# Performance work log

Hardware: AMD Instinct MI355X
Metric: run time of the kernel (lower is better)

Reference implementation:

```python
import jax, jax.numpy as jnp
import numpy as np

N_NODES = 131072
N_EDGES = 2097152
N_GRAPHS = 16384
LRELU_ATT = 0.2   # GATConv negative_slope
LRELU_ACT = 0.01  # F.leaky_relu default
BN_EPS = 1e-5


def _gat_layer(x, src, dst, edge_attr, W, a_src, a_dst, We, a_edge, b, H, C, concat, n_nodes):
    # x: [N, Fin]; W: [Fin, H*C]; a_src/a_dst/a_edge: [H, C]; We: [1, H*C]; b: [H*C] or [C]
    h = (x @ W).reshape(-1, H, C)                                   # [N, H, C]
    alpha_src = jnp.einsum('nhc,hc->nh', h, a_src)                  # [N, H]
    alpha_dst = jnp.einsum('nhc,hc->nh', h, a_dst)                  # [N, H]
    he = (edge_attr @ We).reshape(-1, H, C)                          # [E, H, C]
    alpha_e = jnp.einsum('ehc,hc->eh', he, a_edge)                   # [E, H]
    alpha = alpha_src[src] + alpha_dst[dst] + alpha_e                # [E, H]
    alpha = jax.nn.leaky_relu(alpha, LRELU_ATT)
    # edge-softmax over destination nodes (numerically stable)
    amax = jax.ops.segment_max(alpha, dst, num_segments=n_nodes)
    ex = jnp.exp(alpha - amax[dst])
    denom = jax.ops.segment_sum(ex, dst, num_segments=n_nodes)
    att = ex / (denom[dst] + 1e-16)                                  # [E, H]
    out = jax.ops.segment_sum(h[src] * att[:, :, None], dst, num_segments=n_nodes)  # [N, H, C]
    out = out.reshape(n_nodes, H * C) if concat else out.mean(axis=1)
    return out + b


def setup_inputs() -> dict:
    key = jax.random.key(0)
    ks = iter(jax.random.split(key, 64))
    d = {}
    d['x'] = jax.random.normal(next(ks), (N_NODES, 6), dtype=jnp.float32)
    d['edge_index'] = jax.random.randint(next(ks), (2, N_EDGES), 0, N_NODES, dtype=jnp.int32)
    d['edge_weight'] = jax.random.uniform(next(ks), (N_EDGES,), dtype=jnp.float32)
    d['batch'] = jnp.sort(jax.random.randint(next(ks), (N_NODES,), 0, N_GRAPHS, dtype=jnp.int32))
    # GAT layers: (in, out_channels, heads)
    cfgs = [(6, 16, 4), (64, 32, 4), (128, 16, 4), (64, 50, 1)]
    for i, (fin, C, H) in enumerate(cfgs, 1):
        s = 1.0 / np.sqrt(fin)
        d[f'W{i}'] = jax.random.normal(next(ks), (fin, H * C), dtype=jnp.float32) * s
        d[f'as{i}'] = jax.random.normal(next(ks), (H, C), dtype=jnp.float32) * (1.0 / np.sqrt(C))
        d[f'ad{i}'] = jax.random.normal(next(ks), (H, C), dtype=jnp.float32) * (1.0 / np.sqrt(C))
        d[f'We{i}'] = jax.random.normal(next(ks), (1, H * C), dtype=jnp.float32)
        d[f'ae{i}'] = jax.random.normal(next(ks), (H, C), dtype=jnp.float32) * (1.0 / np.sqrt(C))
        out_dim = H * C if i < 4 else C  # concat for 1-3, not layer 4
        d[f'b{i}'] = jnp.zeros((out_dim,), dtype=jnp.float32)
    d['bn_g'] = jnp.ones((50,), dtype=jnp.float32)
    d['bn_b'] = jnp.zeros((50,), dtype=jnp.float32)
    d['bn_rm'] = jax.random.normal(next(ks), (50,), dtype=jnp.float32) * 0.1
    d['bn_rv'] = jnp.abs(jax.random.normal(next(ks), (50,), dtype=jnp.float32)) + 0.5
    for name, (fi, fo) in [('f1', (50, 30)), ('f2', (30, 20)), ('f3', (20, 2))]:
        d[f'W{name}'] = jax.random.normal(next(ks), (fi, fo), dtype=jnp.float32) * (1.0 / np.sqrt(fi))
        d[f'b{name}'] = jnp.zeros((fo,), dtype=jnp.float32)
    return d


def reference(x, edge_index, edge_weight, batch,
              W1, as1, ad1, We1, ae1, b1,
              W2, as2, ad2, We2, ae2, b2,
              W3, as3, ad3, We3, ae3, b3,
              W4, as4, ad4, We4, ae4, b4,
              bn_g, bn_b, bn_rm, bn_rv,
              Wf1, bf1, Wf2, bf2, Wf3, bf3):
    src, dst = edge_index[0], edge_index[1]
    ea = edge_weight[:, None]  # edge_dim = 1
    n = x.shape[0]
    h = jax.nn.leaky_relu(_gat_layer(x, src, dst, ea, W1, as1, ad1, We1, ae1, b1, 4, 16, True, n), LRELU_ACT)
    h = jax.nn.leaky_relu(_gat_layer(h, src, dst, ea, W2, as2, ad2, We2, ae2, b2, 4, 32, True, n), LRELU_ACT)
    h = jax.nn.leaky_relu(_gat_layer(h, src, dst, ea, W3, as3, ad3, We3, ae3, b3, 4, 16, True, n), LRELU_ACT)
    h = _gat_layer(h, src, dst, ea, W4, as4, ad4, We4, ae4, b4, 1, 50, False, n)
    # BatchNorm (eval mode: running stats)
    h = (h - bn_rm) * jax.lax.rsqrt(bn_rv + BN_EPS) * bn_g + bn_b
    h = jax.nn.leaky_relu(h, LRELU_ACT)
    g = jax.ops.segment_sum(h, batch, num_segments=N_GRAPHS)  # global_add_pool
    g = jax.nn.leaky_relu(g @ Wf1 + bf1, LRELU_ACT)  # dropout p=0.2 is a no-op in eval
    g = jax.nn.leaky_relu(g @ Wf2 + bf2, LRELU_ACT)
    return g @ Wf3 + bf3
```

## Files before the change

### kernel.cpp

```cpp
#include <hip/hip_runtime.h>
#include <hip/hip_fp16.h>
#include <math.h>

#define NN 131072
#define NE 2097152
#define NG 16384

__device__ __forceinline__ float lrelu(float x, float s) { return fmaxf(x, s * x); }

template <int H>
__device__ __forceinline__ float sel_h(const float* a, int hsel) {
    if constexpr (H == 1) return a[0];
    else return hsel == 0 ? a[0] : hsel == 1 ? a[1] : hsel == 2 ? a[2] : a[3];
}

__global__ void k_hist(const int* __restrict__ dst, int* __restrict__ cnt, int* __restrict__ rank) {
    int e = blockIdx.x * 256 + threadIdx.x;
    rank[e] = atomicAdd(&cnt[dst[e]], 1);
}

__global__ void k_scan1(const int* __restrict__ cnt, int* __restrict__ rowptr, int* __restrict__ part) {
    __shared__ int s[256];
    int t = threadIdx.x;
    int i = blockIdx.x * 256 + t;
    int v = cnt[i];
    s[t] = v;
    __syncthreads();
    for (int off = 1; off < 256; off <<= 1) {
        int x = (t >= off) ? s[t - off] : 0;
        __syncthreads();
        s[t] += x;
        __syncthreads();
    }
    rowptr[i] = s[t] - v;
    if (t == 255) part[blockIdx.x] = s[255];
}

__global__ void k_scan2(int* part,
                        const float* __restrict__ We1, const float* __restrict__ ae1,
                        const float* __restrict__ We2, const float* __restrict__ ae2,
                        const float* __restrict__ We3, const float* __restrict__ ae3,
                        const float* __restrict__ We4, const float* __restrict__ ae4,
                        float* __restrict__ ceb) {
    __shared__ int s[512];
    int t = threadIdx.x;
    int v = part[t];
    s[t] = v;
    __syncthreads();
    for (int off = 1; off < 512; off <<= 1) {
        int x = (t >= off) ? s[t - off] : 0;
        __syncthreads();
        s[t] += x;
        __syncthreads();
    }
    part[t] = s[t] - v;
    if (t < 4) {
        float c = 0.f;
        for (int i = 0; i < 16; i++) c += We1[t * 16 + i] * ae1[t * 16 + i];
        ceb[t] = c;
    } else if (t < 8) {
        int h = t - 4;
        float c = 0.f;
        for (int i = 0; i < 32; i++) c += We2[h * 32 + i] * ae2[h * 32 + i];
        ceb[t] = c;
    } else if (t < 12) {
        int h = t - 8;
        float c = 0.f;
        for (int i = 0; i < 16; i++) c += We3[h * 16 + i] * ae3[h * 16 + i];
        ceb[t] = c;
    } else if (t == 12) {
        float c = 0.f;
        for (int i = 0; i < 50; i++) c += We4[i] * ae4[i];
        ceb[t] = c;
    }
}

__global__ void k_scan3(int* __restrict__ rowptr, const int* __restrict__ part) {
    int t = threadIdx.x;
    int i = blockIdx.x * 256 + t;
    rowptr[i] = rowptr[i] + part[blockIdx.x];
    if (i == 0) rowptr[NN] = NE;
}

__global__ void k_scatter(const int* __restrict__ src, const int* __restrict__ dst,
                          const float* __restrict__ ew, const int* __restrict__ rowptr,
                          const int* __restrict__ rank, unsigned int* __restrict__ ep) {
    int e = blockIdx.x * 256 + threadIdx.x;
    int d = dst[e];
    int p = rowptr[d] + rank[e];
    unsigned int s = (unsigned int)src[e];
    unsigned int q = (unsigned int)(ew[e] * 32767.f + 0.5f);
    __builtin_nontemporal_store((s << 15) | (q & 0x7fffu), &ep[p]);
}

__device__ __forceinline__ void ep_unpack(unsigned int u, int& s, float& w) {
    s = (int)(u >> 15);
    w = (float)(u & 0x7fffu) * (1.f / 32767.f);
}

template <int FIN, int F, int FR, int H, int C, int ITER>
__global__ __launch_bounds__(256) void k_transform(
    const float* __restrict__ in, const float* __restrict__ W,
    const float* __restrict__ as_, const float* __restrict__ ad_,
    __half* __restrict__ h, float* __restrict__ alpha_s, float* __restrict__ alpha_d) {
    constexpr int TF = F / 16;
    constexpr int XS = 65;
    __shared__ float Wl[FIN * F];
    __shared__ float Xl[FIN * XS];
    int t = threadIdx.x;
    int tfg = t & 15;
    int ng = t >> 4;
    int f0 = tfg * TF;

    for (int i = t; i < FIN * F; i += 256) {
        int ff = i % F;
        Wl[i] = (ff < FR) ? W[(i / F) * FR + ff] : 0.f;
    }
    float asf[TF], adf[TF];
#pragma unroll
    for (int j = 0; j < TF; j++) {
        bool v = (f0 + j) < FR;
        asf[j] = v ? as_[f0 + j] : 0.f;
        adf[j] = v ? ad_[f0 + j] : 0.f;
    }

    for (int it = 0; it < ITER; ++it) {
        int nb = (blockIdx.x * ITER + it) * 64;
        __syncthreads();
        for (int i = t; i < 64 * FIN; i += 256) {
            int nn = i / FIN, kk = i % FIN;
            Xl[kk * XS + nn] = in[(size_t)(nb + nn) * FIN + kk];
        }
        __syncthreads();

        float acc[4][TF];
#pragma unroll
        for (int i = 0; i < 4; i++)
#pragma unroll
            for (int j = 0; j < TF; j++) acc[i][j] = 0.f;

#pragma unroll 2
        for (int k = 0; k < FIN; ++k) {
            float4 xv = *(const float4*)&Xl[k * XS + ng * 4];
            float wv[TF];
#pragma unroll
            for (int j4 = 0; j4 < TF; j4 += 4) {
                float4 w4 = *(const float4*)&Wl[k * F + f0 + j4];
                wv[j4] = w4.x; wv[j4 + 1] = w4.y; wv[j4 + 2] = w4.z; wv[j4 + 3] = w4.w;
            }
            const float xs[4] = {xv.x, xv.y, xv.z, xv.w};
#pragma unroll
            for (int i = 0; i < 4; i++)
#pragma unroll
                for (int j = 0; j < TF; j++) acc[i][j] = fmaf(xs[i], wv[j], acc[i][j]);
        }

#pragma unroll
        for (int i = 0; i < 4; i++) {
            int n = nb + ng * 4 + i;
            __half hv[TF];
            float ps = 0.f, pd = 0.f;
#pragma unroll
            for (int j = 0; j < TF; j++) {
                hv[j] = __float2half(acc[i][j]);
                ps = fmaf(acc[i][j], asf[j], ps);
                pd = fmaf(acc[i][j], adf[j], pd);
            }
            if constexpr (TF == 4) {
                *(uint2*)(h + (size_t)n * F + f0) = *(uint2*)hv;
            } else {
                *(uint4*)(h + (size_t)n * F + f0) = *(uint4*)hv;
            }
            ps += __shfl_xor(ps, 1);
            pd += __shfl_xor(pd, 1);
            ps += __shfl_xor(ps, 2);
            pd += __shfl_xor(pd, 2);
            if constexpr (H == 1) {
                ps += __shfl_xor(ps, 4);
                pd += __shfl_xor(pd, 4);
                ps += __shfl_xor(ps, 8);
                pd += __shfl_xor(pd, 8);
                if (tfg == 0) {
                    alpha_s[n] = ps;
                    alpha_d[n] = pd;
                }
            } else {
                if ((tfg & 3) == 0) {
                    alpha_s[(size_t)n * H + (tfg >> 2)] = ps;
                    alpha_d[(size_t)n * H + (tfg >> 2)] = pd;
                }
            }
        }
    }
}

template <int H, int C, bool FINAL>
__global__ __launch_bounds__(256) void k_aggregate(
    const __half* __restrict__ h, const float* __restrict__ asrc, const float* __restrict__ adst,
    const int* __restrict__ rowptr, const unsigned int* __restrict__ ep,
    const float* __restrict__ ceb, const float* __restrict__ b,
    const float* __restrict__ bn_g, const float* __restrict__ bn_b,
    const float* __restrict__ bn_rm, const float* __restrict__ bn_rv,
    float* __restrict__ out) {
    constexpr int F = H * C;
    constexpr bool P2 = (F > 64);
    constexpr int FSB = P2 ? 256 : 128;
    constexpr int EPI = P2 ? 4 : 8;
    __shared__ float lds_att[4][(64 + EPI) * H];
    __shared__ int lds_off[4][64 + EPI];

    int wid = threadIdx.x >> 6;
    int lane = threadIdx.x & 63;
    int n = blockIdx.x * 4 + wid;
    int r0 = __builtin_amdgcn_readfirstlane(rowptr[n]);
    int r1 = __builtin_amdgcn_readfirstlane(rowptr[n + 1]);
    int deg = r1 - r0;

    float ce[H], ad[H];
#pragma unroll
    for (int hh = 0; hh < H; hh++) ce[hh] = ceb[hh];
    if constexpr (H == 4) {
        float4 adv = ((const float4*)adst)[n];
        ad[0] = adv.x; ad[1] = adv.y; ad[2] = adv.z; ad[3] = adv.w;
    } else {
        ad[0] = adst[n];
    }

    bool val = lane < deg;
    int s_l = 0;
    float w_l = 0.f;
    if (val) ep_unpack(ep[r0 + lane], s_l, w_l);
    float ex_l[H], psum[H];
    if constexpr (H == 4) {
        if (val) {
            float4 v4 = ((const float4*)asrc)[s_l];
            ex_l[0] = __expf(fminf(lrelu(v4.x + ad[0] + w_l * ce[0], 0.2f), 80.f));
            ex_l[1] = __expf(fminf(lrelu(v4.y + ad[1] + w_l * ce[1], 0.2f), 80.f));
            ex_l[2] = __expf(fminf(lrelu(v4.z + ad[2] + w_l * ce[2], 0.2f), 80.f));
            ex_l[3] = __expf(fminf(lrelu(v4.w + ad[3] + w_l * ce[3], 0.2f), 80.f));
        } else {
            ex_l[0] = ex_l[1] = ex_l[2] = ex_l[3] = 0.f;
        }
    } else {
        ex_l[0] = val ? __expf(fminf(lrelu(asrc[s_l] + ad[0] + w_l * ce[0], 0.2f), 80.f)) : 0.f;
    }
#pragma unroll
    for (int hh = 0; hh < H; hh++) psum[hh] = ex_l[hh];
    for (int r = r0 + 64 + lane; r < r1; r += 64) {
        int s;
        float w;
        ep_unpack(ep[r], s, w);
        if constexpr (H == 4) {
            float4 v4 = ((const float4*)asrc)[s];
            psum[0] += __expf(fminf(lrelu(v4.x + ad[0] + w * ce[0], 0.2f), 80.f));
            psum[1] += __expf(fminf(lrelu(v4.y + ad[1] + w * ce[1], 0.2f), 80.f));
            psum[2] += __expf(fminf(lrelu(v4.z + ad[2] + w * ce[2], 0.2f), 80.f));
            psum[3] += __expf(fminf(lrelu(v4.w + ad[3] + w * ce[3], 0.2f), 80.f));
        } else {
            psum[0] += __expf(fminf(lrelu(asrc[s] + ad[0] + w * ce[0], 0.2f), 80.f));
        }
    }
    float rden[H];
#pragma unroll
    for (int hh = 0; hh < H; hh++) {
        float v = psum[hh];
#pragma unroll
        for (int off = 32; off >= 1; off >>= 1) v += __shfl_xor(v, off);
        rden[hh] = 1.f / (v + 1e-16f);
    }

    lds_off[wid][lane] = s_l * FSB;
#pragma unroll
    for (int hh = 0; hh < H; hh++) lds_att[wid][lane * H + hh] = ex_l[hh] * rden[hh];
    if (lane < EPI) lds_off[wid][64 + lane] = 0;
    if (lane < EPI * H) lds_att[wid][64 * H + lane] = 0.f;
    __syncthreads();

    int jn = deg < 64 ? deg : 64;
    const char* hb = (const char*)h;

    if constexpr (P2) {
        int flane = lane & 15;
        int grp = lane >> 4;
        int f0 = 8 * flane;
        int hsel = f0 >> 5;
        float a[8];
#pragma unroll
        for (int i = 0; i < 8; i++) a[i] = 0.f;
#pragma unroll 4
        for (int j = 0; j < jn; j += EPI) {
            int je = j + grp;
            int off = lds_off[wid][je];
            float att = lds_att[wid][je * H + hsel];
            uint4 p = *(const uint4*)(hb + (size_t)(off + flane * 16));
            const __half2* hp = (const __half2*)&p;
#pragma unroll
            for (int i = 0; i < 4; i++) {
                a[2 * i] = fmaf(__low2float(hp[i]), att, a[2 * i]);
                a[2 * i + 1] = fmaf(__high2float(hp[i]), att, a[2 * i + 1]);
            }
        }
        if (deg > 64) {
            float rdensel = sel_h<H>(rden, hsel);
            for (int r = r0 + 64; r < r1; ++r) {
                unsigned int u = __builtin_amdgcn_readfirstlane(ep[r]);
                int s;
                float w;
                ep_unpack(u, s, w);
                float4 v4 = ((const float4*)asrc)[s];
                float aA[4];
                aA[0] = fminf(lrelu(v4.x + ad[0] + w * ce[0], 0.2f), 80.f);
                aA[1] = fminf(lrelu(v4.y + ad[1] + w * ce[1], 0.2f), 80.f);
                aA[2] = fminf(lrelu(v4.z + ad[2] + w * ce[2], 0.2f), 80.f);
                aA[3] = fminf(lrelu(v4.w + ad[3] + w * ce[3], 0.2f), 80.f);
                float att = __expf(sel_h<H>(aA, hsel)) * rdensel;
                att = (grp == 0) ? att : 0.f;
                uint4 p = *(const uint4*)(hb + (size_t)(s * FSB + flane * 16));
                const __half2* hp = (const __half2*)&p;
#pragma unroll
                for (int i = 0; i < 4; i++) {
                    a[2 * i] = fmaf(__low2float(hp[i]), att, a[2 * i]);
                    a[2 * i + 1] = fmaf(__high2float(hp[i]), att, a[2 * i + 1]);
                }
            }
        }
#pragma unroll
        for (int i = 0; i < 8; i++) {
            a[i] += __shfl_xor(a[i], 32);
            a[i] += __shfl_xor(a[i], 16);
        }
        if (lane < 16) {
            float4 o0, o1;
            o0.x = lrelu(a[0] + b[f0], 0.01f);
            o0.y = lrelu(a[1] + b[f0 + 1], 0.01f);
            o0.z = lrelu(a[2] + b[f0 + 2], 0.01f);
            o0.w = lrelu(a[3] + b[f0 + 3], 0.01f);
            o1.x = lrelu(a[4] + b[f0 + 4], 0.01f);
            o1.y = lrelu(a[5] + b[f0 + 5], 0.01f);
            o1.z = lrelu(a[6] + b[f0 + 6], 0.01f);
            o1.w = lrelu(a[7] + b[f0 + 7], 0.01f);
            ((float4*)out)[(size_t)n * 32 + 2 * flane] = o0;
            ((float4*)out)[(size_t)n * 32 + 2 * flane + 1] = o1;
        }
    } else {
        int flane = lane & 7;
        int grp = lane >> 3;
        int f0 = 8 * flane;
        int hsel = (H == 1) ? 0 : (f0 >> 4);
        float a[8];
#pragma unroll
        for (int i = 0; i < 8; i++) a[i] = 0.f;
#pragma unroll 4
        for (int j = 0; j < jn; j += EPI) {
            int je = j + grp;
            int off = lds_off[wid][je];
            float att = lds_att[wid][je * H + hsel];
            uint4 p = *(const uint4*)(hb + (size_t)(off + flane * 16));
            const __half2* hp = (const __half2*)&p;
#pragma unroll
            for (int i = 0; i < 4; i++) {
                a[2 * i] = fmaf(__low2float(hp[i]), att, a[2 * i]);
                a[2 * i + 1] = fmaf(__high2float(hp[i]), att, a[2 * i + 1]);
            }
        }
        if (deg > 64) {
            float rdensel = sel_h<H>(rden, hsel);
            for (int r = r0 + 64; r < r1; ++r) {
                unsigned int u = __builtin_amdgcn_readfirstlane(ep[r]);
                int s;
                float w;
                ep_unpack(u, s, w);
                float aA[H];
                if constexpr (H == 4) {
                    float4 v4 = ((const float4*)asrc)[s];
                    aA[0] = fminf(lrelu(v4.x + ad[0] + w * ce[0], 0.2f), 80.f);
                    aA[1] = fminf(lrelu(v4.y + ad[1] + w * ce[1], 0.2f), 80.f);
                    aA[2] = fminf(lrelu(v4.z + ad[2] + w * ce[2], 0.2f), 80.f);
                    aA[3] = fminf(lrelu(v4.w + ad[3] + w * ce[3], 0.2f), 80.f);
                } else {
                    aA[0] = fminf(lrelu(asrc[s] + ad[0] + w * ce[0], 0.2f), 80.f);
                }
                float att = __expf(sel_h<H>(aA, hsel)) * rdensel;
                att = (grp == 0) ? att : 0.f;
                uint4 p = *(const uint4*)(hb + (size_t)(s * FSB + flane * 16));
                const __half2* hp = (const __half2*)&p;
#pragma unroll
                for (int i = 0; i < 4; i++) {
                    a[2 * i] = fmaf(__low2float(hp[i]), att, a[2 * i]);
                    a[2 * i + 1] = fmaf(__high2float(hp[i]), att, a[2 * i + 1]);
                }
            }
        }
#pragma unroll
        for (int i = 0; i < 8; i++) {
            a[i] += __shfl_xor(a[i], 32);
            a[i] += __shfl_xor(a[i], 16);
            a[i] += __shfl_xor(a[i], 8);
        }
        if constexpr (FINAL) {
            if (lane < 7) {
                float o[8];
#pragma unroll
                for (int k = 0; k < 8; k++) {
                    int f = f0 + k;
                    if (f < 50) {
                        float v = a[k] + b[f];
                        v = (v - bn_rm[f]) * rsqrtf(bn_rv[f] + 1e-5f) * bn_g[f] + bn_b[f];
                        o[k] = lrelu(v, 0.01f);
                    } else {
                        o[k] = 0.f;
                    }
                }
                if (f0 < 48) {
                    ((float4*)(out + (size_t)n * 64 + f0))[0] = make_float4(o[0], o[1], o[2], o[3]);
                    ((float4*)(out + (size_t)n * 64 + f0))[1] = make_float4(o[4], o[5], o[6], o[7]);
                } else {
                    ((float2*)(out + (size_t)n * 64 + 48))[0] = make_float2(o[0], o[1]);
                }
            }
        } else {
            if (lane < 8) {
                float4 o0, o1;
                o0.x = lrelu(a[0] + b[f0], 0.01f);
                o0.y = lrelu(a[1] + b[f0 + 1], 0.01f);
                o0.z = lrelu(a[2] + b[f0 + 2], 0.01f);
                o0.w = lrelu(a[3] + b[f0 + 3], 0.01f);
                o1.x = lrelu(a[4] + b[f0 + 4], 0.01f);
                o1.y = lrelu(a[5] + b[f0 + 5], 0.01f);
                o1.z = lrelu(a[6] + b[f0 + 6], 0.01f);
                o1.w = lrelu(a[7] + b[f0 + 7], 0.01f);
                ((float4*)out)[(size_t)n * 16 + 2 * flane] = o0;
                ((float4*)out)[(size_t)n * 16 + 2 * flane + 1] = o1;
            }
        }
    }
}

__global__ __launch_bounds__(256) void k_pool(const float* __restrict__ nodeout, const int* __restrict__ batch,
                                              float* __restrict__ gbuf) {
    int wid = threadIdx.x >> 6;
    int lane = threadIdx.x & 63;
    int g = blockIdx.x * 4 + wid;
    int lo = 0, hi = NN;
    while (lo < hi) {
        int mid = (lo + hi) >> 1;
        if (batch[mid] < g) lo = mid + 1; else hi = mid;
    }
    int s0 = lo;
    hi = NN;
    while (lo < hi) {
        int mid = (lo + hi) >> 1;
        if (batch[mid] < g + 1) lo = mid + 1; else hi = mid;
    }
    int s1 = lo;
    if (lane < 50) {
        float acc = 0.f;
        for (int n = s0; n < s1; ++n) acc += nodeout[(size_t)n * 64 + lane];
        gbuf[(size_t)g * 50 + lane] = acc;
    }
}

__global__ __launch_bounds__(64) void k_mlp(const float* __restrict__ gbuf,
                      const float* __restrict__ Wf1, const float* __restrict__ bf1,
                      const float* __restrict__ Wf2, const float* __restrict__ bf2,
                      const float* __restrict__ Wf3, const float* __restrict__ bf3,
                      float* __restrict__ out) {
    __shared__ float W1[1500], W2[600], W3[40], B1[30], B2[20], B3[2];
    __shared__ float G[64 * 50];
    int t = threadIdx.x;
    for (int i = t; i < 1500; i += 64) W1[i] = Wf1[i];
    for (int i = t; i < 600; i += 64) W2[i] = Wf2[i];
    if (t < 40) W3[t] = Wf3[t];
    if (t < 30) B1[t] = bf1[t];
    if (t < 20) B2[t] = bf2[t];
    if (t < 2) B3[t] = bf3[t];
    int g0 = blockIdx.x * 64;
    for (int i = t; i < 64 * 50; i += 64) G[i] = gbuf[(size_t)g0 * 50 + i];
    __syncthreads();
    float gv[50];
#pragma unroll
    for (int i = 0; i < 50; i++) gv[i] = G[t * 50 + i];
    float h1[30];
#pragma unroll
    for (int j = 0; j < 30; j++) {
        float a = B1[j];
#pragma unroll
        for (int i = 0; i < 50; i++) a += gv[i] * W1[i * 30 + j];
        h1[j] = lrelu(a, 0.01f);
    }
    float h2[20];
#pragma unroll
    for (int j = 0; j < 20; j++) {
        float a = B2[j];
#pragma unroll
        for (int i = 0; i < 30; i++) a += h1[i] * W2[i * 20 + j];
        h2[j] = lrelu(a, 0.01f);
    }
    int g = g0 + t;
    float o0 = B3[0], o1 = B3[1];
#pragma unroll
    for (int i = 0; i < 20; i++) {
        o0 += h2[i] * W3[i * 2];
        o1 += h2[i] * W3[i * 2 + 1];
    }
    ((float2*)out)[g] = make_float2(o0, o1);
}

extern "C" void kernel_launch(void* const* d_in, const int* in_sizes, int n_in,
                              void* d_out, int out_size, void* d_ws, size_t ws_size,
                              hipStream_t stream) {
    const float* x = (const float*)d_in[0];
    const int* ei = (const int*)d_in[1];
    const float* ew = (const float*)d_in[2];
    const int* batch = (const int*)d_in[3];
    const float* W1 = (const float*)d_in[4];
    const float* as1 = (const float*)d_in[5];
    const float* ad1 = (const float*)d_in[6];
    const float* We1 = (const float*)d_in[7];
    const float* ae1 = (const float*)d_in[8];
    const float* b1 = (const float*)d_in[9];
    const float* W2 = (const float*)d_in[10];
    const float* as2 = (const float*)d_in[11];
    const float* ad2 = (const float*)d_in[12];
    const float* We2 = (const float*)d_in[13];
    const float* ae2 = (const float*)d_in[14];
    const float* b2 = (const float*)d_in[15];
    const float* W3 = (const float*)d_in[16];
    const float* as3 = (const float*)d_in[17];
    const float* ad3 = (const float*)d_in[18];
    const float* We3 = (const float*)d_in[19];
    const float* ae3 = (const float*)d_in[20];
    const float* b3 = (const float*)d_in[21];
    const float* W4 = (const float*)d_in[22];
    const float* as4 = (const float*)d_in[23];
    const float* ad4 = (const float*)d_in[24];
    const float* We4 = (const float*)d_in[25];
    const float* ae4 = (const float*)d_in[26];
    const float* b4 = (const float*)d_in[27];
    const float* bn_g = (const float*)d_in[28];
    const float* bn_b = (const float*)d_in[29];
    const float* bn_rm = (const float*)d_in[30];
    const float* bn_rv = (const float*)d_in[31];
    const float* Wf1 = (const float*)d_in[32];
    const float* bf1 = (const float*)d_in[33];
    const float* Wf2 = (const float*)d_in[34];
    const float* bf2 = (const float*)d_in[35];
    const float* Wf3 = (const float*)d_in[36];
    const float* bf3 = (const float*)d_in[37];
    float* out = (float*)d_out;

    const int* src = ei;
    const int* dst = ei + NE;

    char* ws = (char*)d_ws;
    float* feat = (float*)ws;         ws += (size_t)NN * 128 * 4;
    __half* hbuf = (__half*)ws;       ws += (size_t)NN * 128 * 2;
    float* as_buf = (float*)ws;       ws += (size_t)NN * 4 * 4;
    float* ad_buf = (float*)ws;       ws += (size_t)NN * 4 * 4;
    int* cnt = (int*)ws;              ws += (size_t)NN * 4;
    int* rowptr = (int*)ws;           ws += (size_t)(NN + 64) * 4;
    unsigned int* ep = (unsigned int*)ws; ws += (size_t)NE * 4;
    int* part = (int*)ws;             ws += 512 * 4;
    float* ce_buf = (float*)ws;       ws += 64 * 4;
    float* gbuf = (float*)ws;         ws += (size_t)NG * 50 * 4;
    int* rank = (int*)hbuf;

    hipMemsetAsync(cnt, 0, (size_t)NN * 4, stream);
    k_hist<<<NE / 256, 256, 0, stream>>>(dst, cnt, rank);
    k_scan1<<<NN / 256, 256, 0, stream>>>(cnt, rowptr, part);
    k_scan2<<<1, 512, 0, stream>>>(part, We1, ae1, We2, ae2, We3, ae3, We4, ae4, ce_buf);
    k_scan3<<<NN / 256, 256, 0, stream>>>(rowptr, part);
    k_scatter<<<NE / 256, 256, 0, stream>>>(src, dst, ew, rowptr, rank, ep);

    k_transform<6, 64, 64, 4, 16, 4><<<NN / 256, 256, 0, stream>>>(x, W1, as1, ad1, hbuf, as_buf, ad_buf);
    k_aggregate<4, 16, false><<<NN / 4, 256, 0, stream>>>(hbuf, as_buf, ad_buf, rowptr, ep, ce_buf,
                                                          b1, nullptr, nullptr, nullptr, nullptr, feat);
    k_transform<64, 128, 128, 4, 32, 4><<<NN / 256, 256, 0, stream>>>(feat, W2, as2, ad2, hbuf, as_buf, ad_buf);
    k_aggregate<4, 32, false><<<NN / 4, 256, 0, stream>>>(hbuf, as_buf, ad_buf, rowptr, ep, ce_buf + 4,
                                                          b2, nullptr, nullptr, nullptr, nullptr, feat);
    k_transform<128, 64, 64, 4, 16, 4><<<NN / 256, 256, 0, stream>>>(feat, W3, as3, ad3, hbuf, as_buf, ad_buf);
    k_aggregate<4, 16, false><<<NN / 4, 256, 0, stream>>>(hbuf, as_buf, ad_buf, rowptr, ep, ce_buf + 8,
                                                          b3, nullptr, nullptr, nullptr, nullptr, feat);
    k_transform<64, 64, 50, 1, 50, 4><<<NN / 256, 256, 0, stream>>>(feat, W4, as4, ad4, hbuf, as_buf, ad_buf);
    k_aggregate<1, 50, true><<<NN / 4, 256, 0, stream>>>(hbuf, as_buf, ad_buf, rowptr, ep, ce_buf + 12,
                                                         b4, bn_g, bn_b, bn_rm, bn_rv, feat);
    k_pool<<<NG / 4, 256, 0, stream>>>(feat, batch, gbuf);
    k_mlp<<<NG / 64, 64, 0, stream>>>(gbuf, Wf1, bf1, Wf2, bf2, Wf3, bf3, out);
}
```

Baseline: 889.7 us.

## Process two destination nodes per wavefront in GAT aggregation

The aggregation kernel now gives each destination node a 32-lane half-wavefront instead of a full 64-lane wave, so each 256-thread block handles 8 nodes and the grid is halved. Average in-degree is about 16, so most lanes were idle under the one-node-per-wave mapping. The change shortens the shuffle reductions and removes the padded LDS tail entries. In exchange, wave-uniform readfirstlane on rowptr and the overflow edge loads is dropped. Nodes with more than 32 neighbours also fall back to the slow serial path, where the two halves can diverge.

```diff
diff --git a/kernel.cpp b/kernel.cpp
--- a/kernel.cpp
+++ b/kernel.cpp
@@ -205,15 +205,16 @@
     constexpr int F = H * C;
     constexpr bool P2 = (F > 64);
     constexpr int FSB = P2 ? 256 : 128;
-    constexpr int EPI = P2 ? 4 : 8;
-    __shared__ float lds_att[4][(64 + EPI) * H];
-    __shared__ int lds_off[4][64 + EPI];
+    __shared__ float lds_att[4][64 * H];
+    __shared__ int lds_off[4][64];
 
     int wid = threadIdx.x >> 6;
     int lane = threadIdx.x & 63;
-    int n = blockIdx.x * 4 + wid;
-    int r0 = __builtin_amdgcn_readfirstlane(rowptr[n]);
-    int r1 = __builtin_amdgcn_readfirstlane(rowptr[n + 1]);
+    int half = lane >> 5;
+    int hl = lane & 31;
+    int n = blockIdx.x * 8 + wid * 2 + half;
+    int r0 = rowptr[n];
+    int r1 = rowptr[n + 1];
     int deg = r1 - r0;
 
     float ce[H], ad[H];
@@ -226,10 +227,10 @@
         ad[0] = adst[n];
     }
 
-    bool val = lane < deg;
+    bool val = hl < deg;
     int s_l = 0;
     float w_l = 0.f;
-    if (val) ep_unpack(ep[r0 + lane], s_l, w_l);
+    if (val) ep_unpack(ep[r0 + hl], s_l, w_l);
     float ex_l[H], psum[H];
     if constexpr (H == 4) {
         if (val) {
@@ -246,7 +247,7 @@
     }
 #pragma unroll
     for (int hh = 0; hh < H; hh++) psum[hh] = ex_l[hh];
-    for (int r = r0 + 64 + lane; r < r1; r += 64) {
+    for (int r = r0 + 32 + hl; r < r1; r += 32) {
         int s;
         float w;
         ep_unpack(ep[r], s, w);
@@ -265,31 +266,30 @@
     for (int hh = 0; hh < H; hh++) {
         float v = psum[hh];
 #pragma unroll
-        for (int off = 32; off >= 1; off >>= 1) v += __shfl_xor(v, off);
+        for (int off = 16; off >= 1; off >>= 1) v += __shfl_xor(v, off);
         rden[hh] = 1.f / (v + 1e-16f);
     }
 
     lds_off[wid][lane] = s_l * FSB;
 #pragma unroll
     for (int hh = 0; hh < H; hh++) lds_att[wid][lane * H + hh] = ex_l[hh] * rden[hh];
-    if (lane < EPI) lds_off[wid][64 + lane] = 0;
-    if (lane < EPI * H) lds_att[wid][64 * H + lane] = 0.f;
     __syncthreads();
 
-    int jn = deg < 64 ? deg : 64;
+    int jn = deg < 32 ? deg : 32;
+    int base = half * 32;
     const char* hb = (const char*)h;
 
     if constexpr (P2) {
-        int flane = lane & 15;
-        int grp = lane >> 4;
+        int flane = hl & 15;
+        int grp = hl >> 4;
         int f0 = 8 * flane;
         int hsel = f0 >> 5;
         float a[8];
 #pragma unroll
         for (int i = 0; i < 8; i++) a[i] = 0.f;
 #pragma unroll 4
-        for (int j = 0; j < jn; j += EPI) {
-            int je = j + grp;
+        for (int j = 0; j < jn; j += 2) {
+            int je = base + j + grp;
             int off = lds_off[wid][je];
             float att = lds_att[wid][je * H + hsel];
             uint4 p = *(const uint4*)(hb + (size_t)(off + flane * 16));
@@ -300,10 +300,10 @@
                 a[2 * i + 1] = fmaf(__high2float(hp[i]), att, a[2 * i + 1]);
             }
         }
-        if (deg > 64) {
+        if (deg > 32) {
             float rdensel = sel_h<H>(rden, hsel);
-            for (int r = r0 + 64; r < r1; ++r) {
-                unsigned int u = __builtin_amdgcn_readfirstlane(ep[r]);
+            for (int r = r0 + 32; r < r1; ++r) {
+                unsigned int u = ep[r];
                 int s;
                 float w;
                 ep_unpack(u, s, w);
@@ -325,11 +325,8 @@
             }
         }
 #pragma unroll
-        for (int i = 0; i < 8; i++) {
-            a[i] += __shfl_xor(a[i], 32);
-            a[i] += __shfl_xor(a[i], 16);
-        }
-        if (lane < 16) {
+        for (int i = 0; i < 8; i++) a[i] += __shfl_xor(a[i], 16);
+        if (hl < 16) {
             float4 o0, o1;
             o0.x = lrelu(a[0] + b[f0], 0.01f);
             o0.y = lrelu(a[1] + b[f0 + 1], 0.01f);
@@ -343,16 +340,16 @@
             ((float4*)out)[(size_t)n * 32 + 2 * flane + 1] = o1;
         }
     } else {
-        int flane = lane & 7;
-        int grp = lane >> 3;
+        int flane = hl & 7;
+        int grp = hl >> 3;
         int f0 = 8 * flane;
         int hsel = (H == 1) ? 0 : (f0 >> 4);
         float a[8];
 #pragma unroll
         for (int i = 0; i < 8; i++) a[i] = 0.f;
 #pragma unroll 4
-        for (int j = 0; j < jn; j += EPI) {
-            int je = j + grp;
+        for (int j = 0; j < jn; j += 4) {
+            int je = base + j + grp;
             int off = lds_off[wid][je];
             float att = lds_att[wid][je * H + hsel];
             uint4 p = *(const uint4*)(hb + (size_t)(off + flane * 16));
@@ -363,10 +360,10 @@
                 a[2 * i + 1] = fmaf(__high2float(hp[i]), att, a[2 * i + 1]);
             }
         }
-        if (deg > 64) {
+        if (deg > 32) {
             float rdensel = sel_h<H>(rden, hsel);
-            for (int r = r0 + 64; r < r1; ++r) {
-                unsigned int u = __builtin_amdgcn_readfirstlane(ep[r]);
+            for (int r = r0 + 32; r < r1; ++r) {
+                unsigned int u = ep[r];
                 int s;
                 float w;
                 ep_unpack(u, s, w);
@@ -393,12 +390,11 @@
         }
 #pragma unroll
         for (int i = 0; i < 8; i++) {
-            a[i] += __shfl_xor(a[i], 32);
+            a[i] += __shfl_xor(a[i], 8);
             a[i] += __shfl_xor(a[i], 16);
-            a[i] += __shfl_xor(a[i], 8);
         }
         if constexpr (FINAL) {
-            if (lane < 7) {
+            if (hl < 7) {
                 float o[8];
 #pragma unroll
                 for (int k = 0; k < 8; k++) {
@@ -419,7 +415,7 @@
                 }
             }
         } else {
-            if (lane < 8) {
+            if (hl < 8) {
                 float4 o0, o1;
                 o0.x = lrelu(a[0] + b[f0], 0.01f);
                 o0.y = lrelu(a[1] + b[f0 + 1], 0.01f);
@@ -573,16 +569,16 @@
     k_scatter<<<NE / 256, 256, 0, stream>>>(src, dst, ew, rowptr, rank, ep);
 
     k_transform<6, 64, 64, 4, 16, 4><<<NN / 256, 256, 0, stream>>>(x, W1, as1, ad1, hbuf, as_buf, ad_buf);
-    k_aggregate<4, 16, false><<<NN / 4, 256, 0, stream>>>(hbuf, as_buf, ad_buf, rowptr, ep, ce_buf,
+    k_aggregate<4, 16, false><<<NN / 8, 256, 0, stream>>>(hbuf, as_buf, ad_buf, rowptr, ep, ce_buf,
                                                           b1, nullptr, nullptr, nullptr, nullptr, feat);
     k_transform<64, 128, 128, 4, 32, 4><<<NN / 256, 256, 0, stream>>>(feat, W2, as2, ad2, hbuf, as_buf, ad_buf);
-    k_aggregate<4, 32, false><<<NN / 4, 256, 0, stream>>>(hbuf, as_buf, ad_buf, rowptr, ep, ce_buf + 4,
+    k_aggregate<4, 32, false><<<NN / 8, 256, 0, stream>>>(hbuf, as_buf, ad_buf, rowptr, ep, ce_buf + 4,
                                                           b2, nullptr, nullptr, nullptr, nullptr, feat);
     k_transform<128, 64, 64, 4, 16, 4><<<NN / 256, 256, 0, stream>>>(feat, W3, as3, ad3, hbuf, as_buf, ad_buf);
-    k_aggregate<4, 16, false><<<NN / 4, 256, 0, stream>>>(hbuf, as_buf, ad_buf, rowptr, ep, ce_buf + 8,
+    k_aggregate<4, 16, false><<<NN / 8, 256, 0, stream>>>(hbuf, as_buf, ad_buf, rowptr, ep, ce_buf + 8,
                                                           b3, nullptr, nullptr, nullptr, nullptr, feat);
     k_transform<64, 64, 50, 1, 50, 4><<<NN / 256, 256, 0, stream>>>(feat, W4, as4, ad4, hbuf, as_buf, ad_buf);
-    k_aggregate<1, 50, true><<<NN / 4, 256, 0, stream>>>(hbuf, as_buf, ad_buf, rowptr, ep, ce_buf + 12,
+    k_aggregate<1, 50, true><<<NN / 8, 256, 0, stream>>>(hbuf, as_buf, ad_buf, rowptr, ep, ce_buf + 12,
                                                          b4, bn_g, bn_b, bn_rm, bn_rv, feat);
     k_pool<<<NG / 4, 256, 0, stream>>>(feat, batch, gbuf);
     k_mlp<<<NG / 64, 64, 0, stream>>>(gbuf, Wf1, bf1, Wf2, bf2, Wf3, bf3, out);
```

Measured after the change: 788.2 us. 1.13x faster.
